# Kernel optimization log

Measured on AMD Instinct MI355X. Metric: run time of the kernel, lower is better.

The kernel has to match this reference:

```python
import jax, jax.numpy as jnp
import numpy as np

NUM_CLASSES = 50000
FEATURE_DIM = 512
BATCH = 4096
NUM_INTERNAL = NUM_CLASSES - 1
TREE_DEPTH = int(np.ceil(np.log2(NUM_CLASSES)))  # 16


def _build_path_maps():
    # Replicates the __init__ loop: for each class leaf, walk to root.
    path_nodes = np.full((NUM_CLASSES, TREE_DEPTH), -1, dtype=np.int32)
    path_dirs = np.full((NUM_CLASSES, TREE_DEPTH), -1, dtype=np.int32)
    for c in range(NUM_CLASSES):
        curr = NUM_INTERNAL + c
        nodes, dirs = [], []
        while curr > 0:
            parent = (curr - 1) // 2
            nodes.append(parent)
            dirs.append((curr - 1) % 2)
            curr = parent
        L = len(nodes)
        path_nodes[c, :L] = nodes[::-1]
        path_dirs[c, :L] = dirs[::-1]
    return jnp.asarray(path_nodes), jnp.asarray(path_dirs)


def setup_inputs() -> dict:
    key = jax.random.key(0)
    k1, k2, k3 = jax.random.split(key, 3)
    features = jax.random.normal(k1, (BATCH, FEATURE_DIM), dtype=jnp.float32)
    targets = jax.random.randint(k2, (BATCH, 1), 0, NUM_CLASSES, dtype=jnp.int32)
    # glorot_uniform over (NUM_INTERNAL, FEATURE_DIM, 2): fan_in=FEATURE_DIM, fan_out=2
    limit = float(np.sqrt(6.0 / (FEATURE_DIM + 2)))
    node_weights = jax.random.uniform(k3, (NUM_INTERNAL, FEATURE_DIM, 2),
                                      minval=-limit, maxval=limit, dtype=jnp.float32)
    path_nodes_map, path_directions_map = _build_path_maps()
    return {"features": features, "targets": targets, "node_weights": node_weights,
            "path_nodes_map": path_nodes_map, "path_directions_map": path_directions_map}


def reference(features, targets, node_weights, path_nodes_map, path_directions_map):
    targets_flat = jnp.squeeze(targets.astype(jnp.int32), axis=-1)          # [B]
    batch_path_nodes = jnp.take(path_nodes_map, targets_flat, axis=0)       # [B, K]
    batch_path_dirs = jnp.take(path_directions_map, targets_flat, axis=0)   # [B, K]
    mask = (batch_path_nodes != -1).astype(features.dtype)                  # [B, K]
    safe_nodes = jnp.where(batch_path_nodes == -1, 0, batch_path_nodes)
    path_weights = jnp.take(node_weights, safe_nodes, axis=0)               # [B, K, D, 2]
    node_logits = jnp.einsum('bd,bkdc->bkc', features, path_weights)        # [B, K, 2]
    node_log_probs = jax.nn.log_softmax(node_logits, axis=-1)               # [B, K, 2]
    safe_dirs = jnp.where(batch_path_dirs == -1, 0, batch_path_dirs)
    selected = jnp.take_along_axis(node_log_probs, safe_dirs[..., None], axis=-1)[..., 0]
    total_log_prob = jnp.sum(selected * mask, axis=-1)                      # [B]
    return -total_log_prob
```

## Files before the change

### kernel.cpp

```cpp
#include <hip/hip_runtime.h>
#include <math.h>


constexpr int BATCH = 4096;
constexpr int FDIM  = 512;
constexpr int DEPTH = 16;

__global__ __launch_bounds__(256) void hstree_loss(
    const float* __restrict__ features,
    const int*   __restrict__ targets,
    const float* __restrict__ node_weights,
    const int*   __restrict__ path_nodes,
    const int*   __restrict__ path_dirs,
    float*       __restrict__ out)
{
    const int lane = threadIdx.x & 63;
    const int b    = (blockIdx.x << 2) + (threadIdx.x >> 6);
    if (b >= BATCH) return;

    const int t = __builtin_amdgcn_readfirstlane(targets[b]);

    int nodes[DEPTH];
    int dirs[DEPTH];
#pragma unroll
    for (int k = 0; k < DEPTH; ++k) {
        nodes[k] = path_nodes[t * DEPTH + k];
        dirs[k]  = path_dirs [t * DEPTH + k];
    }

    const float4* fb = (const float4*)(features + (size_t)b * FDIM);
    const float4 f0 = fb[lane];
    const float4 f1 = fb[lane + 64];

    auto wbase = [&](int k) -> const float4* {
        int n = nodes[k] < 0 ? 0 : nodes[k];
        return (const float4*)(node_weights + (size_t)n * (FDIM * 2));
    };

    const float4* wp = wbase(0);
    float4 a0 = wp[2 * lane];
    float4 a1 = wp[2 * lane + 1];
    float4 a2 = wp[128 + 2 * lane];
    float4 a3 = wp[128 + 2 * lane + 1];

    float loss = 0.0f;

#pragma unroll 1
    for (int k = 0; k < DEPTH; ++k) {
        const int kn = (k + 1 < DEPTH) ? (k + 1) : k;
        const float4* np = wbase(kn);
        float4 b0 = np[2 * lane];
        float4 b1 = np[2 * lane + 1];
        float4 b2 = np[128 + 2 * lane];
        float4 b3 = np[128 + 2 * lane + 1];

        float l0 = f0.x * a0.x + f0.y * a0.z + f0.z * a1.x + f0.w * a1.z
                 + f1.x * a2.x + f1.y * a2.z + f1.z * a3.x + f1.w * a3.z;
        float l1 = f0.x * a0.y + f0.y * a0.w + f0.z * a1.y + f0.w * a1.w
                 + f1.x * a2.y + f1.y * a2.w + f1.z * a3.y + f1.w * a3.w;

#pragma unroll
        for (int off = 32; off; off >>= 1) {
            l0 += __shfl_xor(l0, off, 64);
            l1 += __shfl_xor(l1, off, 64);
        }

        if (nodes[k] >= 0) {
            const float z = (dirs[k] == 0) ? (l0 - l1) : (l1 - l0);
            loss += fmaxf(-z, 0.0f) + log1pf(__expf(-fabsf(z)));
        }

        a0 = b0; a1 = b1; a2 = b2; a3 = b3;
    }

    if (lane == 0) out[b] = loss;
}

extern "C" void kernel_launch(void* const* d_in, const int* in_sizes, int n_in,
                              void* d_out, int out_size, void* d_ws, size_t ws_size,
                              hipStream_t stream) {
    const float* features     = (const float*)d_in[0];
    const int*   targets      = (const int*)  d_in[1];
    const float* node_weights = (const float*)d_in[2];
    const int*   path_nodes   = (const int*)  d_in[3];
    const int*   path_dirs    = (const int*)  d_in[4];
    float*       out          = (float*)d_out;

    hstree_loss<<<BATCH / 4, 256, 0, stream>>>(
        features, targets, node_weights, path_nodes, path_dirs, out);
}
```

Baseline: 264.9 us.

## Map tree levels to lane quads instead of serial per-level wave reductions

Assigns each group of four lanes to one of the sixteen path nodes, so all levels' weight rows are gathered concurrently rather than one level at a time with a single-node prefetch. Each lane accumulates a strided quarter of the dot product, reduces within the quad, then sums the softplus terms across quads. This removes the per-level full-wave shuffle reductions and raises memory-level parallelism, at the cost of narrower per-node coalescing and repeated feature loads per quad.

```diff
diff --git a/kernel.cpp b/kernel.cpp
--- a/kernel.cpp
+++ b/kernel.cpp
@@ -16,64 +16,54 @@
 {
     const int lane = threadIdx.x & 63;
     const int b    = (blockIdx.x << 2) + (threadIdx.x >> 6);
-    if (b >= BATCH) return;
+
+    const int k = lane >> 2;
+    const int q = lane & 3;
 
     const int t = __builtin_amdgcn_readfirstlane(targets[b]);
 
-    int nodes[DEPTH];
-    int dirs[DEPTH];
-#pragma unroll
-    for (int k = 0; k < DEPTH; ++k) {
-        nodes[k] = path_nodes[t * DEPTH + k];
-        dirs[k]  = path_dirs [t * DEPTH + k];
+    const int node = path_nodes[t * DEPTH + k];
+    const int dir  = path_dirs [t * DEPTH + k];
+    const int n    = node < 0 ? 0 : node;
+
+    const float4* __restrict__ wp = (const float4*)(node_weights + (size_t)n * (FDIM * 2)) + 2 * q;
+    const float4* __restrict__ fp = (const float4*)(features + (size_t)b * FDIM) + q;
+
+    float acc0a = 0.f, acc1a = 0.f, acc0b = 0.f, acc1b = 0.f;
+
+#pragma unroll 4
+    for (int j = 0; j < 32; j += 2) {
+        const float4 wa0 = wp[8 * j];
+        const float4 wb0 = wp[8 * j + 1];
+        const float4 f0  = fp[4 * j];
+        const float4 wa1 = wp[8 * j + 8];
+        const float4 wb1 = wp[8 * j + 9];
+        const float4 f1  = fp[4 * j + 4];
+
+        acc0a += f0.x * wa0.x + f0.y * wa0.z + f0.z * wb0.x + f0.w * wb0.z;
+        acc1a += f0.x * wa0.y + f0.y * wa0.w + f0.z * wb0.y + f0.w * wb0.w;
+        acc0b += f1.x * wa1.x + f1.y * wa1.z + f1.z * wb1.x + f1.w * wb1.z;
+        acc1b += f1.x * wa1.y + f1.y * wa1.w + f1.z * wb1.y + f1.w * wb1.w;
     }
 
-    const float4* fb = (const float4*)(features + (size_t)b * FDIM);
-    const float4 f0 = fb[lane];
-    const float4 f1 = fb[lane + 64];
+    float l0 = acc0a + acc0b;
+    float l1 = acc1a + acc1b;
 
-    auto wbase = [&](int k) -> const float4* {
-        int n = nodes[k] < 0 ? 0 : nodes[k];
-        return (const float4*)(node_weights + (size_t)n * (FDIM * 2));
-    };
+    l0 += __shfl_xor(l0, 1, 64);
+    l1 += __shfl_xor(l1, 1, 64);
+    l0 += __shfl_xor(l0, 2, 64);
+    l1 += __shfl_xor(l1, 2, 64);
 
-    const float4* wp = wbase(0);
-    float4 a0 = wp[2 * lane];
-    float4 a1 = wp[2 * lane + 1];
-    float4 a2 = wp[128 + 2 * lane];
-    float4 a3 = wp[128 + 2 * lane + 1];
+    const float z  = (dir == 0) ? (l0 - l1) : (l1 - l0);
+    const float sp = fmaxf(-z, 0.0f) + log1pf(__expf(-fabsf(z)));
 
-    float loss = 0.0f;
+    float v = (node >= 0 && q == 0) ? sp : 0.0f;
+    v += __shfl_xor(v, 4, 64);
+    v += __shfl_xor(v, 8, 64);
+    v += __shfl_xor(v, 16, 64);
+    v += __shfl_xor(v, 32, 64);
 
-#pragma unroll 1
-    for (int k = 0; k < DEPTH; ++k) {
-        const int kn = (k + 1 < DEPTH) ? (k + 1) : k;
-        const float4* np = wbase(kn);
-        float4 b0 = np[2 * lane];
-        float4 b1 = np[2 * lane + 1];
-        float4 b2 = np[128 + 2 * lane];
-        float4 b3 = np[128 + 2 * lane + 1];
-
-        float l0 = f0.x * a0.x + f0.y * a0.z + f0.z * a1.x + f0.w * a1.z
-                 + f1.x * a2.x + f1.y * a2.z + f1.z * a3.x + f1.w * a3.z;
-        float l1 = f0.x * a0.y + f0.y * a0.w + f0.z * a1.y + f0.w * a1.w
-                 + f1.x * a2.y + f1.y * a2.w + f1.z * a3.y + f1.w * a3.w;
-
-#pragma unroll
-        for (int off = 32; off; off >>= 1) {
-            l0 += __shfl_xor(l0, off, 64);
-            l1 += __shfl_xor(l1, off, 64);
-        }
-
-        if (nodes[k] >= 0) {
-            const float z = (dirs[k] == 0) ? (l0 - l1) : (l1 - l0);
-            loss += fmaxf(-z, 0.0f) + log1pf(__expf(-fabsf(z)));
-        }
-
-        a0 = b0; a1 = b1; a2 = b2; a3 = b3;
-    }
-
-    if (lane == 0) out[b] = loss;
+    if (lane == 0) out[b] = v;
 }
 
 extern "C" void kernel_launch(void* const* d_in, const int* in_sizes, int n_in,
```

Measured after the change: 266.9 us. No clear change (+0.8%).
